# Optimization experiments

Hardware: AMD Instinct MI355X
Metric: run time of the kernel (lower is better)

## Reference

```python
import jax, jax.numpy as jnp
import numpy as np

L, H, P_LOC = 32768, 512, 256  # seq len, in/out dim, local state dim (conj_sym: P//2)
DT_MIN, DT_MAX = 1e-3, 1e-1
STEP_RESCALE = 1.0


def setup_inputs() -> dict:
    key = jax.random.key(0)
    ks = jax.random.split(key, 10)
    # stable eigenvalues: negative real part (mimics HiPPO init real part -1/2)
    Lambda_re = -0.1 - jax.random.uniform(ks[0], (P_LOC,), dtype=jnp.float32)
    Lambda_im = jax.random.normal(ks[1], (P_LOC,), dtype=jnp.float32) * jnp.pi
    B_re = jax.random.normal(ks[2], (P_LOC, H), dtype=jnp.float32) / jnp.sqrt(2.0 * H)
    B_im = jax.random.normal(ks[3], (P_LOC, H), dtype=jnp.float32) / jnp.sqrt(2.0 * H)
    C_re = jax.random.normal(ks[4], (H, P_LOC), dtype=jnp.float32) / jnp.sqrt(2.0 * P_LOC)
    C_im = jax.random.normal(ks[5], (H, P_LOC), dtype=jnp.float32) / jnp.sqrt(2.0 * P_LOC)
    D = jax.random.normal(ks[6], (H,), dtype=jnp.float32)
    u01 = jax.random.uniform(ks[7], (P_LOC,), dtype=jnp.float32)
    log_step = u01 * (jnp.log(DT_MAX) - jnp.log(DT_MIN)) + jnp.log(DT_MIN)
    input_sequence = jax.random.normal(ks[8], (L, H), dtype=jnp.float32)
    integration_timesteps = jax.random.uniform(ks[9], (L,), dtype=jnp.float32)
    return {
        "input_sequence": input_sequence,
        "integration_timesteps": integration_timesteps,
        "Lambda_re": Lambda_re, "Lambda_im": Lambda_im,
        "B_re": B_re, "B_im": B_im,
        "C_re": C_re, "C_im": C_im,
        "D": D, "log_step": log_step,
    }


def _binop(q_i, q_j):
    A_i, b_i = q_i
    A_j, b_j = q_j
    return (A_j * A_i, A_j * b_i + b_j)


def reference(input_sequence, integration_timesteps, Lambda_re, Lambda_im,
              B_re, B_im, C_re, C_im, D, log_step):
    Lambda = Lambda_re + 1j * Lambda_im          # (P,)
    B = B_re + 1j * B_im                         # (P, H)
    C_tilde = C_re + 1j * C_im                   # (H, P)
    step = STEP_RESCALE * jnp.exp(log_step)      # (P,)
    # ZOH discretization per timestep: Delta[l,p] = step[p] * dt[l]
    Delta = integration_timesteps[:, None] * step[None, :]          # (L, P)
    Lambda_bar = jnp.exp(Lambda[None, :] * Delta)                   # (L, P) complex
    gamma_bar = (Lambda_bar - 1.0) / Lambda[None, :]                # (L, P) complex
    Bu = gamma_bar * jnp.einsum("lh,ph->lp", input_sequence.astype(B.dtype), B)
    _, xs = jax.lax.associative_scan(_binop, (Lambda_bar, Bu))      # (L, P)
    # conj_sym=True -> output is 2 * Re(C x)
    ys = 2.0 * jnp.einsum("lp,hp->lh", xs, C_tilde).real            # (L, H)
    return ys + D[None, :] * input_sequence
```

## Files before the change

kernel.cpp:

```cpp
#include <hip/hip_runtime.h>
#include <math.h>

#define L_SEQ 32768
#define H_DIM 512
#define P_DIM 256
#define K_DIM 512
#define CHUNK 32
#define NCHUNK (L_SEQ / CHUNK)

typedef __bf16 bf16x8 __attribute__((ext_vector_type(8)));
typedef float floatx4 __attribute__((ext_vector_type(4)));

__device__ __forceinline__ void gll16(const void* g, void* l) {
    __builtin_amdgcn_global_load_lds(
        (__attribute__((address_space(1))) void*)(g),
        (__attribute__((address_space(3))) void*)(l), 16, 0, 0);
}

__global__ __launch_bounds__(512) void build_kernel(
    const float* __restrict__ Bre, const float* __restrict__ Bim,
    const float* __restrict__ Cre, const float* __restrict__ Cim,
    __bf16* __restrict__ B2, __bf16* __restrict__ C2)
{
    const int b = blockIdx.x;
    const int t = threadIdx.x;
    if (b < 256) {
        B2[(2 * b) * 512 + t]     = (__bf16)Bre[b * H_DIM + t];
        B2[(2 * b + 1) * 512 + t] = (__bf16)Bim[b * H_DIM + t];
    } else {
        const int h = b - 256;
        const int p = t & 255;
        if (t < 256)
            C2[h * 512 + 2 * p]     = (__bf16)Cre[h * P_DIM + p];
        else
            C2[h * 512 + 2 * p + 1] = (__bf16)(-Cim[h * P_DIM + p]);
    }
}

__global__ __launch_bounds__(256) void gemm1_kernel(
    const float* __restrict__ A,
    const __bf16* __restrict__ Bm,
    __bf16* __restrict__ Out)
{
    __shared__ float  Asf[128 * 32];
    __shared__ __bf16 Bs [128 * 32];

    const int tid = threadIdx.x;
    const int w  = tid >> 6;
    const int ln = tid & 63;
    const int bm = blockIdx.x;
    const int bn = blockIdx.y;

    floatx4 acc[4][4];
    #pragma unroll
    for (int i = 0; i < 4; ++i)
        #pragma unroll
        for (int j = 0; j < 4; ++j)
            acc[i][j] = (floatx4){0.f, 0.f, 0.f, 0.f};

    const int a_r = ln >> 3;
    const int a_c = (ln & 7) << 2;
    const int b_r = ln >> 2;
    const int b_c = (ln & 3) << 3;
    const size_t brow = (size_t)(bn * 128 + w * 16 + b_r) * K_DIM;

    float*  lA[4];
    size_t  gAr[4];
    #pragma unroll
    for (int q = 0; q < 4; ++q) {
        lA[q] = Asf + (q * 32 + w * 8) * 32;
        gAr[q] = (size_t)(bm * 128 + q * 32 + w * 8 + a_r) * K_DIM;
    }
    __bf16* lB0 = Bs + w * 512;
    __bf16* lB1 = Bs + 2048 + w * 512;

    const int wm = (w >> 1) * 64;
    const int wn = (w & 1) * 64;
    const int fr = ln & 15;
    const int fq = (ln >> 4) * 8;

    for (int kt = 0; kt < K_DIM; kt += 32) {
        __syncthreads();
        #pragma unroll
        for (int q = 0; q < 4; ++q)
            gll16(A + gAr[q] + kt + a_c, lA[q]);
        gll16(Bm + brow + kt + b_c,                      lB0);
        gll16(Bm + brow + (size_t)64 * K_DIM + kt + b_c, lB1);
        __syncthreads();

        bf16x8 a[4], b[4];
        #pragma unroll
        for (int mt = 0; mt < 4; ++mt) {
            floatx4 a0 = *(floatx4*)&Asf[(wm + mt * 16 + fr) * 32 + fq];
            floatx4 a1 = *(floatx4*)&Asf[(wm + mt * 16 + fr) * 32 + fq + 4];
            #pragma unroll
            for (int r = 0; r < 4; ++r) {
                a[mt][r]     = (__bf16)a0[r];
                a[mt][4 + r] = (__bf16)a1[r];
            }
        }
        #pragma unroll
        for (int nt = 0; nt < 4; ++nt)
            b[nt] = *(bf16x8*)&Bs[(wn + nt * 16 + fr) * 32 + fq];

        #pragma unroll
        for (int mt = 0; mt < 4; ++mt)
            #pragma unroll
            for (int nt = 0; nt < 4; ++nt)
                acc[mt][nt] = __builtin_amdgcn_mfma_f32_16x16x32_bf16(
                    a[mt], b[nt], acc[mt][nt], 0, 0, 0);
    }

    const int rq = (ln >> 4) * 4;
    #pragma unroll
    for (int mt = 0; mt < 4; ++mt) {
        const int gro = bm * 128 + wm + mt * 16 + rq;
        #pragma unroll
        for (int nt = 0; nt < 4; ++nt) {
            const int gco = bn * 128 + wn + nt * 16 + (ln & 15);
            #pragma unroll
            for (int r = 0; r < 4; ++r)
                Out[(size_t)(gro + r) * 512 + gco] = (__bf16)acc[mt][nt][r];
        }
    }
}

__global__ __launch_bounds__(256) void gemm2_kernel(
    const __bf16* __restrict__ A,
    const __bf16* __restrict__ Bm,
    float* __restrict__ Out,
    const float* __restrict__ U,
    const float* __restrict__ Dv)
{
    __shared__ __bf16 As[128 * 32];
    __shared__ __bf16 Bs[128 * 32];

    const int tid = threadIdx.x;
    const int w  = tid >> 6;
    const int ln = tid & 63;
    const int bm = blockIdx.x;
    const int bn = blockIdx.y;

    floatx4 acc[4][4];
    #pragma unroll
    for (int i = 0; i < 4; ++i)
        #pragma unroll
        for (int j = 0; j < 4; ++j)
            acc[i][j] = (floatx4){0.f, 0.f, 0.f, 0.f};

    const int lr = ln >> 2;
    const int lce = (ln & 3) << 3;
    const size_t arow = (size_t)(bm * 128 + w * 16 + lr) * K_DIM;
    const size_t brow = (size_t)(bn * 128 + w * 16 + lr) * K_DIM;

    __bf16* lA0 = As + w * 512;
    __bf16* lA1 = As + 2048 + w * 512;
    __bf16* lB0 = Bs + w * 512;
    __bf16* lB1 = Bs + 2048 + w * 512;

    const int wm = (w >> 1) * 64;
    const int wn = (w & 1) * 64;
    const int fr = ln & 15;
    const int fq = (ln >> 4) * 8;

    for (int kt = 0; kt < K_DIM; kt += 32) {
        __syncthreads();
        gll16(A  + arow + kt + lce,                      lA0);
        gll16(A  + arow + (size_t)64 * K_DIM + kt + lce, lA1);
        gll16(Bm + brow + kt + lce,                      lB0);
        gll16(Bm + brow + (size_t)64 * K_DIM + kt + lce, lB1);
        __syncthreads();

        bf16x8 a[4], b[4];
        #pragma unroll
        for (int mt = 0; mt < 4; ++mt)
            a[mt] = *(bf16x8*)&As[(wm + mt * 16 + fr) * 32 + fq];
        #pragma unroll
        for (int nt = 0; nt < 4; ++nt)
            b[nt] = *(bf16x8*)&Bs[(wn + nt * 16 + fr) * 32 + fq];

        #pragma unroll
        for (int mt = 0; mt < 4; ++mt)
            #pragma unroll
            for (int nt = 0; nt < 4; ++nt)
                acc[mt][nt] = __builtin_amdgcn_mfma_f32_16x16x32_bf16(
                    a[mt], b[nt], acc[mt][nt], 0, 0, 0);
    }

    const int rq = (ln >> 4) * 4;
    #pragma unroll
    for (int mt = 0; mt < 4; ++mt) {
        const int gro = bm * 128 + wm + mt * 16 + rq;
        #pragma unroll
        for (int nt = 0; nt < 4; ++nt) {
            const int gco = bn * 128 + wn + nt * 16 + (ln & 15);
            const float dh = Dv[gco];
            #pragma unroll
            for (int r = 0; r < 4; ++r) {
                const size_t o = (size_t)(gro + r) * 512 + gco;
                Out[o] = 2.0f * acc[mt][nt][r] + dh * U[o];
            }
        }
    }
}

template <int WRITE_X>
__global__ __launch_bounds__(256) void scan_chunk_kernel(
    const float* __restrict__ dts,
    const float* __restrict__ Lre_g, const float* __restrict__ Lim_g,
    const float* __restrict__ logstep,
    unsigned int* __restrict__ G2u,
    float4* __restrict__ Agg,
    const float2* __restrict__ Carry)
{
    const int p = threadIdx.x;
    const int c = blockIdx.x;
    const int base = c * CHUNK;

    unsigned int g[CHUNK];
    float dt[CHUNK];
    #pragma unroll
    for (int i = 0; i < CHUNK; ++i)
        g[i] = G2u[(size_t)(base + i) * 256 + p];
    #pragma unroll
    for (int i = 0; i < CHUNK; ++i)
        dt[i] = dts[base + i];

    const float lre = Lre_g[p];
    const float lim = Lim_g[p];
    const float stp = __expf(logstep[p]);
    const float inv_den = 1.0f / (lre * lre + lim * lim);

    float Are = 1.0f, Aim = 0.0f;
    float xre, xim;
    if (WRITE_X) {
        float2 cc = Carry[c * P_DIM + p];
        xre = cc.x; xim = cc.y;
    } else {
        xre = 0.0f; xim = 0.0f;
    }

    #pragma unroll
    for (int i = 0; i < CHUNK; ++i) {
        const float d = stp * dt[i];
        const float er = __expf(lre * d);
        float sn, cs;
        __sincosf(lim * d, &sn, &cs);
        const float are = er * cs;
        const float aim = er * sn;
        const float am1 = are - 1.0f;
        const float gr = (am1 * lre + aim * lim) * inv_den;
        const float gi = (aim * lre - am1 * lim) * inv_den;

        const float ure = __uint_as_float(g[i] << 16);
        const float uim = __uint_as_float(g[i] & 0xffff0000u);
        const float bre = gr * ure - gi * uim;
        const float bim = gr * uim + gi * ure;

        const float nxre = are * xre - aim * xim + bre;
        const float nxim = are * xim + aim * xre + bim;
        xre = nxre; xim = nxim;

        if (WRITE_X) {
            __bf16 xr = (__bf16)xre;
            __bf16 xi = (__bf16)xim;
            unsigned int o = (unsigned int)*(unsigned short*)&xr |
                             ((unsigned int)*(unsigned short*)&xi << 16);
            G2u[(size_t)(base + i) * 256 + p] = o;
        } else {
            const float nAre = are * Are - aim * Aim;
            const float nAim = are * Aim + aim * Are;
            Are = nAre; Aim = nAim;
        }
    }

    if (!WRITE_X)
        Agg[p * NCHUNK + c] = make_float4(Are, Aim, xre, xim);
}

struct CT { float Ar, Ai, br, bi; };

__device__ __forceinline__ CT ct_compose(const CT& f, const CT& s) {
    CT r;
    r.Ar = s.Ar * f.Ar - s.Ai * f.Ai;
    r.Ai = s.Ar * f.Ai + s.Ai * f.Ar;
    r.br = s.Ar * f.br - s.Ai * f.bi + s.br;
    r.bi = s.Ar * f.bi + s.Ai * f.br + s.bi;
    return r;
}

__global__ __launch_bounds__(256) void carry_shfl_kernel(
    const float4* __restrict__ Agg,
    float2* __restrict__ Carry)
{
    const int pch = blockIdx.x;
    const int t  = threadIdx.x;
    const int ln = t & 63;
    const int wv = t >> 6;

    __shared__ float4 wtot[4];

    CT v[4];
    #pragma unroll
    for (int i = 0; i < 4; ++i) {
        float4 f = Agg[(size_t)pch * NCHUNK + 4 * t + i];
        v[i].Ar = f.x; v[i].Ai = f.y; v[i].br = f.z; v[i].bi = f.w;
    }
    CT val = v[0];
    #pragma unroll
    for (int i = 1; i < 4; ++i) val = ct_compose(val, v[i]);

    #pragma unroll
    for (int off = 1; off < 64; off <<= 1) {
        CT o;
        o.Ar = __shfl_up(val.Ar, off);
        o.Ai = __shfl_up(val.Ai, off);
        o.br = __shfl_up(val.br, off);
        o.bi = __shfl_up(val.bi, off);
        if (ln >= off) val = ct_compose(o, val);
    }

    CT lexcl;
    lexcl.Ar = __shfl_up(val.Ar, 1);
    lexcl.Ai = __shfl_up(val.Ai, 1);
    lexcl.br = __shfl_up(val.br, 1);
    lexcl.bi = __shfl_up(val.bi, 1);
    if (ln == 0) { lexcl.Ar = 1.f; lexcl.Ai = 0.f; lexcl.br = 0.f; lexcl.bi = 0.f; }

    if (ln == 63) wtot[wv] = make_float4(val.Ar, val.Ai, val.br, val.bi);
    __syncthreads();

    CT wpre; wpre.Ar = 1.f; wpre.Ai = 0.f; wpre.br = 0.f; wpre.bi = 0.f;
    for (int i = 0; i < wv; ++i) {
        float4 f = wtot[i];
        CT tt; tt.Ar = f.x; tt.Ai = f.y; tt.br = f.z; tt.bi = f.w;
        wpre = ct_compose(wpre, tt);
    }

    CT E = ct_compose(wpre, lexcl);
    #pragma unroll
    for (int i = 0; i < 4; ++i) {
        Carry[(size_t)(4 * t + i) * P_DIM + pch] = make_float2(E.br, E.bi);
        E = ct_compose(E, v[i]);
    }
}

extern "C" void kernel_launch(void* const* d_in, const int* in_sizes, int n_in,
                              void* d_out, int out_size, void* d_ws, size_t ws_size,
                              hipStream_t stream) {
    const float* U       = (const float*)d_in[0];
    const float* dts     = (const float*)d_in[1];
    const float* Lre     = (const float*)d_in[2];
    const float* Lim     = (const float*)d_in[3];
    const float* Bre     = (const float*)d_in[4];
    const float* Bim     = (const float*)d_in[5];
    const float* Cre     = (const float*)d_in[6];
    const float* Cim     = (const float*)d_in[7];
    const float* Dv      = (const float*)d_in[8];
    const float* logstep = (const float*)d_in[9];
    float* out = (float*)d_out;

    char* ws = (char*)d_ws;
    __bf16* G2 = (__bf16*)ws;
    __bf16* B2 = (__bf16*)(ws + (size_t)L_SEQ * 512 * 2);
    __bf16* C2 = B2 + 512 * 512;
    float4* Agg = (float4*)(C2 + 512 * 512);
    float2* Carry = (float2*)(Agg + (size_t)P_DIM * NCHUNK);

    build_kernel<<<768, 512, 0, stream>>>(Bre, Bim, Cre, Cim, B2, C2);

    dim3 g1(L_SEQ / 128, 4);
    gemm1_kernel<<<g1, 256, 0, stream>>>(U, B2, G2);

    unsigned int* G2u = (unsigned int*)G2;
    scan_chunk_kernel<0><<<NCHUNK, 256, 0, stream>>>(
        dts, Lre, Lim, logstep, G2u, Agg, nullptr);
    carry_shfl_kernel<<<P_DIM, 256, 0, stream>>>(Agg, Carry);
    scan_chunk_kernel<1><<<NCHUNK, 256, 0, stream>>>(
        dts, Lre, Lim, logstep, G2u, nullptr, Carry);

    dim3 g2(L_SEQ / 128, 4);
    gemm2_kernel<<<g2, 256, 0, stream>>>(G2, C2, out, U, Dv);
}
```

Baseline: 228.3 us.

## Enlarge gemm2 tiles to 256x256 with double-buffered 64-wide K stages

```diff
diff --git a/kernel.cpp b/kernel.cpp
--- a/kernel.cpp
+++ b/kernel.cpp
@@ -125,15 +125,15 @@
     }
 }
 
-__global__ __launch_bounds__(256) void gemm2_kernel(
+__global__ __launch_bounds__(512, 2) void gemm2_kernel(
     const __bf16* __restrict__ A,
     const __bf16* __restrict__ Bm,
     float* __restrict__ Out,
     const float* __restrict__ U,
     const float* __restrict__ Dv)
 {
-    __shared__ __bf16 As[128 * 32];
-    __shared__ __bf16 Bs[128 * 32];
+    __shared__ __bf16 As[2][256 * 64];
+    __shared__ __bf16 Bs[2][256 * 64];
 
     const int tid = threadIdx.x;
     const int w  = tid >> 6;
@@ -141,59 +141,70 @@
     const int bm = blockIdx.x;
     const int bn = blockIdx.y;
 
-    floatx4 acc[4][4];
-    #pragma unroll
-    for (int i = 0; i < 4; ++i)
+    const int wr = w >> 2;
+    const int wc = w & 3;
+
+    floatx4 acc[8][4];
+    #pragma unroll
+    for (int i = 0; i < 8; ++i)
         #pragma unroll
         for (int j = 0; j < 4; ++j)
             acc[i][j] = (floatx4){0.f, 0.f, 0.f, 0.f};
 
-    const int lr = ln >> 2;
-    const int lce = (ln & 3) << 3;
-    const size_t arow = (size_t)(bm * 128 + w * 16 + lr) * K_DIM;
-    const size_t brow = (size_t)(bn * 128 + w * 16 + lr) * K_DIM;
-
-    __bf16* lA0 = As + w * 512;
-    __bf16* lA1 = As + 2048 + w * 512;
-    __bf16* lB0 = Bs + w * 512;
-    __bf16* lB1 = Bs + 2048 + w * 512;
-
-    const int wm = (w >> 1) * 64;
-    const int wn = (w & 1) * 64;
+    const int srow = ln >> 3;
+    const int scol = (ln & 7) << 3;
+    const size_t agbase = (size_t)(bm * 256 + w * 8 + srow) * K_DIM + scol;
+    const size_t bgbase = (size_t)(bn * 256 + w * 8 + srow) * K_DIM + scol;
+
     const int fr = ln & 15;
-    const int fq = (ln >> 4) * 8;
-
-    for (int kt = 0; kt < K_DIM; kt += 32) {
+    const int fq = (ln >> 4) << 3;
+
+    auto stage = [&](int kt, int buf) {
+        #pragma unroll
+        for (int q = 0; q < 4; ++q) {
+            const int r0 = q * 64 + w * 8;
+            gll16(A  + agbase + (size_t)q * 64 * K_DIM + kt, &As[buf][r0 * 64]);
+            gll16(Bm + bgbase + (size_t)q * 64 * K_DIM + kt, &Bs[buf][r0 * 64]);
+        }
+    };
+    auto compute = [&](int buf) {
+        #pragma unroll
+        for (int ks = 0; ks < 2; ++ks) {
+            bf16x8 a[8], b[4];
+            #pragma unroll
+            for (int mt = 0; mt < 8; ++mt)
+                a[mt] = *(const bf16x8*)
+                    &As[buf][(wr * 128 + mt * 16 + fr) * 64 + ks * 32 + fq];
+            #pragma unroll
+            for (int nt = 0; nt < 4; ++nt)
+                b[nt] = *(const bf16x8*)
+                    &Bs[buf][(wc * 64 + nt * 16 + fr) * 64 + ks * 32 + fq];
+            #pragma unroll
+            for (int mt = 0; mt < 8; ++mt)
+                #pragma unroll
+                for (int nt = 0; nt < 4; ++nt)
+                    acc[mt][nt] = __builtin_amdgcn_mfma_f32_16x16x32_bf16(
+                        a[mt], b[nt], acc[mt][nt], 0, 0, 0);
+        }
+    };
+
+    stage(0, 0);
+    __syncthreads();
+
+    #pragma unroll
+    for (int t = 0; t < 8; ++t) {
+        if (t + 1 < 8) stage((t + 1) * 64, (t + 1) & 1);
+        compute(t & 1);
         __syncthreads();
-        gll16(A  + arow + kt + lce,                      lA0);
-        gll16(A  + arow + (size_t)64 * K_DIM + kt + lce, lA1);
-        gll16(Bm + brow + kt + lce,                      lB0);
-        gll16(Bm + brow + (size_t)64 * K_DIM + kt + lce, lB1);
-        __syncthreads();
-
-        bf16x8 a[4], b[4];
-        #pragma unroll
-        for (int mt = 0; mt < 4; ++mt)
-            a[mt] = *(bf16x8*)&As[(wm + mt * 16 + fr) * 32 + fq];
-        #pragma unroll
-        for (int nt = 0; nt < 4; ++nt)
-            b[nt] = *(bf16x8*)&Bs[(wn + nt * 16 + fr) * 32 + fq];
-
-        #pragma unroll
-        for (int mt = 0; mt < 4; ++mt)
-            #pragma unroll
-            for (int nt = 0; nt < 4; ++nt)
-                acc[mt][nt] = __builtin_amdgcn_mfma_f32_16x16x32_bf16(
-                    a[mt], b[nt], acc[mt][nt], 0, 0, 0);
     }
 
     const int rq = (ln >> 4) * 4;
     #pragma unroll
-    for (int mt = 0; mt < 4; ++mt) {
-        const int gro = bm * 128 + wm + mt * 16 + rq;
+    for (int mt = 0; mt < 8; ++mt) {
+        const int gro = bm * 256 + wr * 128 + mt * 16 + rq;
         #pragma unroll
         for (int nt = 0; nt < 4; ++nt) {
-            const int gco = bn * 128 + wn + nt * 16 + (ln & 15);
+            const int gco = bn * 256 + wc * 64 + nt * 16 + (ln & 15);
             const float dh = Dv[gco];
             #pragma unroll
             for (int r = 0; r < 4; ++r) {
@@ -379,6 +390,6 @@
     scan_chunk_kernel<1><<<NCHUNK, 256, 0, stream>>>(
         dts, Lre, Lim, logstep, G2u, nullptr, Carry);
 
-    dim3 g2(L_SEQ / 128, 4);
-    gemm2_kernel<<<g2, 256, 0, stream>>>(G2, C2, out, U, Dv);
-}
+    dim3 g2(L_SEQ / 256, 2);
+    gemm2_kernel<<<g2, 512, 0, stream>>>(G2, C2, out, U, Dv);
+}
```

Result: slower. 243.3 us (+6.6%).
